# Optimization experiments

Measured on AMD Instinct MI355X. Metric: run time of the kernel, lower is better.

The kernel has to match this reference:

```python
import jax, jax.numpy as jnp
import numpy as np

N, DIM, H, W = 4, 64, 192, 192
K, DIL = 3, 1
STEP = DIL + 1
US = K + DIL * (K - 1)   # effective unfold window = 5
PAD = US // 2
EPS = 1e-5
D4 = DIM // 4


def group_norm(x, gamma, beta, groups=4, eps=EPS):
    n, c = x.shape[0], x.shape[1]
    xg = x.reshape(n, groups, -1)
    m = xg.mean(axis=2, keepdims=True)
    v = xg.var(axis=2, keepdims=True)
    xg = (xg - m) / jnp.sqrt(v + eps)
    xn = xg.reshape(x.shape)
    shp = (1, c) + (1,) * (x.ndim - 2)
    return xn * gamma.reshape(shp) + beta.reshape(shp)


def conv1x1(x, w, b):
    return jnp.einsum('nchw,oc->nohw', x, w) + b.reshape(1, -1, 1, 1)


def dwconv3(x, w, b, dilation):
    c = x.shape[1]
    p = dilation
    y = jax.lax.conv_general_dilated(x, w, (1, 1), [(p, p), (p, p)],
        rhs_dilation=(dilation, dilation), feature_group_count=c,
        dimension_numbers=('NCHW', 'OIHW', 'NCHW'))
    return y + b.reshape(1, -1, 1, 1)


def conv3(x, w, b):
    y = jax.lax.conv_general_dilated(x, w, (1, 1), [(1, 1), (1, 1)],
        dimension_numbers=('NCHW', 'OIHW', 'NCHW'))
    return y + b.reshape(1, -1, 1, 1)


def prelu(x, a):
    return jnp.where(x >= 0, x, a * x)


def forward(x, w_filter, gnf_g, gnf_b,
            lb_w1, lb_b1, lb_a1, lb_dw1, lb_db1,
            lb_w2, lb_b2, lb_a2, lb_dw2, lb_db2,
            lb_w3, lb_b3, lb_a3, lb_dw3, lb_db3,
            lb_w4, lb_b4, lb_a4, lb_w5, lb_b5,
            hb_gn_g, hb_gn_b, hb_w, hb_b,
            fu_w1, fu_b1, fu_gn_g, fu_gn_b, fu_w2, fu_b2):
    n, c, h, w = x.shape
    # dynamic per-channel filter from global average pool (1x1 spatial)
    fp = x.mean(axis=(2, 3))                          # [n, dim]
    fw = fp @ w_filter.T                              # 1x1 conv, no bias -> [n, dim*K*K]
    fw = group_norm(fw[:, :, None, None], gnf_g, gnf_b).reshape(n, DIM, K * K)
    fsm = jax.nn.softmax(fw, axis=2)                  # softmax over the K*K kernel taps
    # masked unfold == gather only the 9 dilated (stride-STEP) taps from reflect-padded x
    xp = jnp.pad(x, ((0, 0), (0, 0), (PAD, PAD), (PAD, PAD)), mode='reflect')
    taps = jnp.stack([xp[:, :, i:i + h, j:j + w]
                      for i in range(0, US, STEP)
                      for j in range(0, US, STEP)], axis=2)   # [n, dim, K*K, h, w]
    low = jnp.einsum('ndkhw,ndk->ndhw', taps, fsm)
    high = x - low
    # low-frequency branch
    y = prelu(conv1x1(low, lb_w1, lb_b1), lb_a1)
    y = dwconv3(y, lb_dw1, lb_db1, 5)
    y = prelu(conv1x1(y, lb_w2, lb_b2), lb_a2)
    y = dwconv3(y, lb_dw2, lb_db2, 1)
    y = prelu(conv1x1(y, lb_w3, lb_b3), lb_a3)
    y = dwconv3(y, lb_dw3, lb_db3, 3)
    y = prelu(conv1x1(y, lb_w4, lb_b4), lb_a4)
    enh_low = conv1x1(y, lb_w5, lb_b5)
    # high-frequency branch (GroupNorm -> LeakyReLU -> 3x3 conv) + residual
    z = group_norm(high, hb_gn_g, hb_gn_b)
    z = jnp.where(z >= 0, z, 0.01 * z)
    enh_high = conv3(z, hb_w, hb_b) + high
    # fusion
    fused = jnp.concatenate([enh_low, enh_high], axis=1)
    o = conv1x1(fused, fu_w1, fu_b1)
    o = group_norm(o, fu_gn_g, fu_gn_b)
    o = jax.nn.gelu(o, approximate=False)
    return conv1x1(o, fu_w2, fu_b2)


def setup_inputs():
    key = jax.random.key(0)
    ks = jax.random.split(key, 16)
    f32 = jnp.float32
    d, d4 = DIM, D4
    rn = lambda k, shape, s=0.05: jax.random.normal(k, shape, dtype=f32) * s
    a = lambda: jnp.array(0.25, f32)   # PReLU init
    return {
        'x': jax.random.normal(ks[0], (N, d, H, W), dtype=f32),
        'w_filter': rn(ks[1], (d * K * K, d)),
        'gnf_g': jnp.ones((d * K * K,), f32), 'gnf_b': jnp.zeros((d * K * K,), f32),
        'lb_w1': rn(ks[2], (d4, d)), 'lb_b1': jnp.zeros((d4,), f32), 'lb_a1': a(),
        'lb_dw1': rn(ks[3], (d4, 1, 3, 3)), 'lb_db1': jnp.zeros((d4,), f32),
        'lb_w2': rn(ks[4], (d4, d4)), 'lb_b2': jnp.zeros((d4,), f32), 'lb_a2': a(),
        'lb_dw2': rn(ks[5], (d4, 1, 3, 3)), 'lb_db2': jnp.zeros((d4,), f32),
        'lb_w3': rn(ks[6], (d4, d4)), 'lb_b3': jnp.zeros((d4,), f32), 'lb_a3': a(),
        'lb_dw3': rn(ks[7], (d4, 1, 3, 3)), 'lb_db3': jnp.zeros((d4,), f32),
        'lb_w4': rn(ks[8], (d4, d4)), 'lb_b4': jnp.zeros((d4,), f32), 'lb_a4': a(),
        'lb_w5': rn(ks[9], (d, d4)), 'lb_b5': jnp.zeros((d,), f32),
        'hb_gn_g': jnp.ones((d,), f32), 'hb_gn_b': jnp.zeros((d,), f32),
        'hb_w': rn(ks[10], (d, d, 3, 3)), 'hb_b': jnp.zeros((d,), f32),
        'fu_w1': rn(ks[11], (2 * d, 2 * d)), 'fu_b1': jnp.zeros((2 * d,), f32),
        'fu_gn_g': jnp.ones((2 * d,), f32), 'fu_gn_b': jnp.zeros((2 * d,), f32),
        'fu_w2': rn(ks[12], (d, 2 * d)), 'fu_b2': jnp.zeros((d,), f32),
    }


def reference(x, w_filter, gnf_g, gnf_b, lb_w1, lb_b1, lb_a1, lb_dw1, lb_db1, lb_w2, lb_b2, lb_a2, lb_dw2, lb_db2, lb_w3, lb_b3, lb_a3, lb_dw3, lb_db3, lb_w4, lb_b4, lb_a4, lb_w5, lb_b5, hb_gn_g, hb_gn_b, hb_w, hb_b, fu_w1, fu_b1, fu_gn_g, fu_gn_b, fu_w2, fu_b2):
    return forward(x, w_filter, gnf_g, gnf_b, lb_w1, lb_b1, lb_a1, lb_dw1, lb_db1, lb_w2, lb_b2, lb_a2, lb_dw2, lb_db2, lb_w3, lb_b3, lb_a3, lb_dw3, lb_db3, lb_w4, lb_b4, lb_a4, lb_w5, lb_b5, hb_gn_g, hb_gn_b, hb_w, hb_b, fu_w1, fu_b1, fu_gn_g, fu_gn_b, fu_w2, fu_b2)
```

## Files before the change

### kernel.cpp

```cpp
#include <hip/hip_runtime.h>
#include <hip/hip_bf16.h>
#include <math.h>

#define Nn 4
#define Cc 64
#define Hh 192
#define Ww 192
#define HW (Hh*Ww)
#define PIXBLK 144

typedef __attribute__((ext_vector_type(4))) float f32x4;
typedef __attribute__((ext_vector_type(8))) short s16x8;

struct __align__(8) US4 { unsigned short x,y,z,w; };

static __device__ __forceinline__ unsigned short f2bf(float v){
    __hip_bfloat16 b = __float2bfloat16(v);
    return *(unsigned short*)&b;
}
static __device__ __forceinline__ float bf2f(unsigned int u){
    return __uint_as_float(u<<16);
}

__global__ void k_prep(const float* __restrict__ hw, const float* __restrict__ fw1,
                       const float* __restrict__ fw2, const float* __restrict__ x,
                       unsigned short* __restrict__ g_wt,
                       unsigned short* __restrict__ g_wfu1,
                       unsigned short* __restrict__ g_wfu2,
                       float* __restrict__ fp){
    int b = blockIdx.x;
    __shared__ float sm[4];
    if(b < 240){
        int idx = b*256 + threadIdx.x;
        if(idx<36864){
            int og = idx/9216, r = idx%9216;
            int t = r/1024, r2 = r%1024;
            int o = r2>>6, c = r2&63;
            g_wt[idx] = f2bf(hw[(size_t)(((og*16+o)*64)+c)*9 + t]);
        } else if(idx<53248){
            int i = idx-36864;
            int o = i>>7, c = i&127;
            g_wfu1[o*128 + (c ^ ((o&15)<<3))] = f2bf(fw1[i]);
        } else {
            int i = idx-53248;
            int o = i>>7, c = i&127;
            g_wfu2[o*128 + (c ^ ((o&15)<<3))] = f2bf(fw2[i]);
        }
    } else {
        int nc = b-240;
        const float4* p = (const float4*)(x + (size_t)nc*HW);
        float s = 0.f;
        for(int i=threadIdx.x;i<HW/4;i+=256){ float4 v=p[i]; s += v.x+v.y+v.z+v.w; }
        for(int o=32;o>0;o>>=1) s += __shfl_down(s,o);
        int wid = threadIdx.x>>6, ln = threadIdx.x&63;
        if(ln==0) sm[wid]=s;
        __syncthreads();
        if(threadIdx.x==0) fp[nc] = (sm[0]+sm[1]+sm[2]+sm[3]) / (float)HW;
    }
}

__global__ void k_filter(const float* __restrict__ fp, const float* __restrict__ wf,
                         const float* __restrict__ gg, const float* __restrict__ gb,
                         float* __restrict__ fsm){
    int n = blockIdx.x;
    __shared__ float sfp[64];
    __shared__ float sfw[576];
    __shared__ float gstat[8];
    int t = threadIdx.x;
    if(t<64) sfp[t] = fp[n*64+t];
    __syncthreads();
    const float* wr = wf + (size_t)t*64;
    float acc = 0.f;
    #pragma unroll 8
    for(int k=0;k<64;k++) acc += sfp[k]*wr[k];
    sfw[t] = acc;
    __syncthreads();
    if(t<4){
        float s=0.f,s2=0.f;
        for(int i=0;i<144;i++){ float v=sfw[t*144+i]; s+=v; s2+=v*v; }
        float m = s/144.f;
        gstat[t*2]   = m;
        gstat[t*2+1] = s2/144.f - m*m;
    }
    __syncthreads();
    int g = t/144;
    float m = gstat[g*2], var = gstat[g*2+1];
    float z = (acc-m)*rsqrtf(var+1e-5f)*gg[t] + gb[t];
    sfw[t] = z;
    __syncthreads();
    if(t<64){
        float mx = -1e30f;
        for(int j=0;j<9;j++) mx = fmaxf(mx, sfw[t*9+j]);
        float e[9]; float se=0.f;
        for(int j=0;j<9;j++){ e[j]=expf(sfw[t*9+j]-mx); se+=e[j]; }
        float inv = 1.f/se;
        for(int j=0;j<9;j++) fsm[((size_t)n*64+t)*9+j] = e[j]*inv;
    }
}

#define HBS 88
__global__ void __launch_bounds__(256,3)
k_lowhigh(const float* __restrict__ x, const float* __restrict__ fsm,
          const float* __restrict__ w1, const float* __restrict__ b1,
          const float* __restrict__ a1p,
          unsigned short* __restrict__ high, float* __restrict__ y1,
          float* __restrict__ partial){
    int bid = blockIdx.x;
    int n = bid/144, tile = bid%144;
    int h0 = (tile/12)*16, w0 = (tile%12)*16;
    int t = threadIdx.x;
    int r0 = t>>4, wl = t&15;
    __shared__ __align__(16) unsigned short highbuf[256*HBS];
    __shared__ float sf[576];
    __shared__ float sw[1024];
    __shared__ float sb[16];
    __shared__ float redsm[4][8];
    for(int i=t;i<576;i+=256) sf[i] = fsm[(size_t)n*576+i];
    for(int i=t;i<1024;i+=256) sw[i] = w1[i];
    if(t<16) sb[t] = b1[t];
    __syncthreads();
    int rh[3], rw[3];
    #pragma unroll
    for(int k=0;k<3;k++){
        int a = h0 + r0 + 2*(k-1); if(a<0) a=-a; if(a>=Hh) a=2*(Hh-1)-a; rh[k]=a;
        int c = w0 + wl + 2*(k-1); if(c<0) c=-c; if(c>=Ww) c=2*(Ww-1)-c; rw[k]=c;
    }
    float acc[16];
    #pragma unroll
    for(int o=0;o<16;o++) acc[o]=0.f;
    const float* xb = x + (size_t)n*Cc*HW;
    int wv = t>>6, ln = t&63;
    #pragma unroll 1
    for(int grp=0; grp<4; grp++){
        float sg=0.f, sq=0.f;
        #pragma unroll 1
        for(int sub=0; sub<2; sub++){
            int oct = grp*2 + sub;
            unsigned int hp[4];
            #pragma unroll
            for(int j=0;j<8;j++){
                int c = oct*8 + j;
                const float* xc = xb + (size_t)c*HW;
                float low=0.f, ctr=0.f;
                #pragma unroll
                for(int ki=0;ki<3;ki++){
                    #pragma unroll
                    for(int kj=0;kj<3;kj++){
                        float v = xc[rh[ki]*Ww + rw[kj]];
                        low += sf[c*9 + ki*3 + kj]*v;
                        if(ki==1 && kj==1) ctr = v;
                    }
                }
                float hv = ctr-low;
                sg += hv; sq += hv*hv;
                unsigned short h16 = f2bf(hv);
                if(j&1) hp[j>>1] |= ((unsigned int)h16)<<16; else hp[j>>1] = h16;
                #pragma unroll
                for(int o=0;o<16;o++) acc[o] += sw[o*64+c]*low;
            }
            uint4 pk; pk.x=hp[0]; pk.y=hp[1]; pk.z=hp[2]; pk.w=hp[3];
            *(uint4*)&highbuf[t*HBS + oct*8] = pk;
        }
        #pragma unroll
        for(int o=32;o>0;o>>=1){ sg+=__shfl_down(sg,o); sq+=__shfl_down(sq,o); }
        if(ln==0){ redsm[wv][grp*2]=sg; redsm[wv][grp*2+1]=sq; }
    }
    float a1 = *a1p;
    #pragma unroll
    for(int o=0;o<16;o++){
        float v = acc[o] + sb[o];
        v = v>=0.f ? v : a1*v;
        y1[((size_t)n*16 + o)*HW + (h0+r0)*Ww + w0 + wl] = v;
    }
    __syncthreads();
    uint4* gout = (uint4*)(high + (size_t)n*HW*64);
    #pragma unroll
    for(int it=0;it<8;it++){
        int i = it*256 + t;
        int px = i>>3, sl = i&7;
        uint4 v = *(const uint4*)&highbuf[px*HBS + sl*8];
        gout[((size_t)(h0+(px>>4))*Ww + w0 + (px&15))*8 + sl] = v;
    }
    if(t<8) partial[(size_t)bid*8 + t] = redsm[0][t]+redsm[1][t]+redsm[2][t]+redsm[3][t];
}

template<int DILT>
__global__ void k_dw_c(const float* __restrict__ yin,
                       const float* __restrict__ dw, const float* __restrict__ db,
                       const float* __restrict__ wc, const float* __restrict__ bc,
                       const float* __restrict__ ap, float* __restrict__ yout){
    int bid = blockIdx.x;
    int n = bid/PIXBLK;
    int pix = (bid%PIXBLK)*256 + threadIdx.x;
    int h = pix/Ww, w = pix%Ww;
    __shared__ float sdw[16*9];
    __shared__ float swc[16*16];
    __shared__ float sdb[16], sbc[16];
    if(threadIdx.x<144) sdw[threadIdx.x] = dw[threadIdx.x];
    if(threadIdx.x>=144 && threadIdx.x<144+16){ sdb[threadIdx.x-144]=db[threadIdx.x-144]; }
    if(threadIdx.x>=160 && threadIdx.x<160+16){ sbc[threadIdx.x-160]=bc[threadIdx.x-160]; }
    for(int i=threadIdx.x;i<256;i+=256) swc[i]=wc[i];
    __syncthreads();
    float t16[16];
    const float* yb = yin + (size_t)n*16*HW;
    for(int c=0;c<16;c++){
        float s = 0.f;
        #pragma unroll
        for(int u=0;u<3;u++){
            int hh = h + DILT*(u-1);
            if(hh<0 || hh>=Hh) continue;
            #pragma unroll
            for(int v=0;v<3;v++){
                int wwi = w + DILT*(v-1);
                if(wwi<0 || wwi>=Ww) continue;
                s += yb[(size_t)c*HW + hh*Ww + wwi]*sdw[c*9+u*3+v];
            }
        }
        t16[c] = s + sdb[c];
    }
    float a = *ap;
    #pragma unroll
    for(int o=0;o<16;o++){
        float s = sbc[o];
        #pragma unroll
        for(int c=0;c<16;c++) s += swc[o*16+c]*t16[c];
        s = s>=0.f ? s : a*s;
        yout[((size_t)n*16 + o)*HW + pix] = s;
    }
}

__global__ void k_dw3_final(const float* __restrict__ yin,
                            const float* __restrict__ dw, const float* __restrict__ db,
                            const float* __restrict__ w4, const float* __restrict__ b4,
                            const float* __restrict__ a4p,
                            const float* __restrict__ w5, const float* __restrict__ b5,
                            unsigned short* __restrict__ enh_low){
    int bid = blockIdx.x;
    int n = bid/PIXBLK;
    int pix = (bid%PIXBLK)*256 + threadIdx.x;
    int h = pix/Ww, w = pix%Ww;
    __shared__ float sdw[16*9];
    __shared__ float sw4[16*16];
    __shared__ float sw5[64*16];
    __shared__ float sdb[16], sb4[16], sb5[64];
    if(threadIdx.x<144) sdw[threadIdx.x]=dw[threadIdx.x];
    if(threadIdx.x<16){ sdb[threadIdx.x]=db[threadIdx.x]; sb4[threadIdx.x]=b4[threadIdx.x]; }
    if(threadIdx.x<64) sb5[threadIdx.x]=b5[threadIdx.x];
    for(int i=threadIdx.x;i<256;i+=256) sw4[i]=w4[i];
    for(int i=threadIdx.x;i<1024;i+=256) sw5[i]=w5[i];
    __syncthreads();
    float t16[16];
    const float* yb = yin + (size_t)n*16*HW;
    for(int c=0;c<16;c++){
        float s=0.f;
        #pragma unroll
        for(int u=0;u<3;u++){
            int hh = h + 3*(u-1);
            if(hh<0||hh>=Hh) continue;
            #pragma unroll
            for(int v=0;v<3;v++){
                int wwi = w + 3*(v-1);
                if(wwi<0||wwi>=Ww) continue;
                s += yb[(size_t)c*HW + hh*Ww + wwi]*sdw[c*9+u*3+v];
            }
        }
        t16[c] = s + sdb[c];
    }
    float a = *a4p;
    float y4[16];
    #pragma unroll
    for(int o=0;o<16;o++){
        float s = sb4[o];
        #pragma unroll
        for(int c=0;c<16;c++) s += sw4[o*16+c]*t16[c];
        y4[o] = s>=0.f ? s : a*s;
    }
    unsigned short* dst = enh_low + ((size_t)n*HW + pix)*64;
    #pragma unroll
    for(int ob=0;ob<64;ob+=4){
        unsigned short tmp[4];
        #pragma unroll
        for(int j=0;j<4;j++){
            int o=ob+j;
            float s = sb5[o];
            #pragma unroll
            for(int c=0;c<16;c++) s += sw5[o*16+c]*y4[c];
            tmp[j]=f2bf(s);
        }
        US4 pk; pk.x=tmp[0]; pk.y=tmp[1]; pk.z=tmp[2]; pk.w=tmp[3];
        *(US4*)&dst[ob] = pk;
    }
}

__global__ void k_redstats(const float* __restrict__ partial, float* __restrict__ st, int nblk){
    int b = blockIdx.x;
    int n = b>>2, gl = b&3;
    int tid = threadIdx.x;
    float a0=0.f, a1=0.f;
    for(int pt=tid; pt<nblk; pt+=256){
        size_t base = (size_t)(n*nblk+pt)*8 + gl*2;
        a0 += partial[base];
        a1 += partial[base+1];
    }
    #pragma unroll
    for(int o=32;o>0;o>>=1){ a0+=__shfl_down(a0,o); a1+=__shfl_down(a1,o); }
    __shared__ float sm[8];
    int wv=tid>>6, ln=tid&63;
    if(ln==0){ sm[wv*2]=a0; sm[wv*2+1]=a1; }
    __syncthreads();
    if(tid==0){
        st[b*32+0] = sm[0]+sm[2]+sm[4]+sm[6];
        st[b*32+1] = sm[1]+sm[3]+sm[5]+sm[7];
    }
}

__global__ void __launch_bounds__(256,3)
k_conv3m(const unsigned short* __restrict__ high, const float* __restrict__ st,
         const float* __restrict__ gng, const float* __restrict__ gnb,
         const unsigned short* __restrict__ g_wt, const float* __restrict__ hb,
         unsigned short* __restrict__ enh_high){
    int bid = blockIdx.x;
    int n = bid/144, tile = bid%144;
    int tr0 = (tile/12)*16, tc0 = (tile%12)*16;
    __shared__ __align__(16) unsigned short z_lds[324*64];
    __shared__ float ssc[64], sbi[64], sbias[64];
    int tid = threadIdx.x;
    if(tid<64){
        int c=tid, g=n*4+(c>>4);
        float cnt=16.f*(float)HW;
        float m=st[g*32]/cnt, var=st[g*32+1]/cnt-m*m;
        float sc=gng[c]*rsqrtf(var+1e-5f);
        ssc[c]=sc; sbi[c]=gnb[c]-m*sc;
        sbias[c]=hb[c];
    }
    __syncthreads();
    const uint4* hpm = (const uint4*)(high + (size_t)n*HW*64);
    for(int e=tid;e<2592;e+=256){
        int hpx = e>>3, q = e&7;
        int hr = hpx/18, hc = hpx - hr*18;
        int gr = tr0+hr-1, gc = tc0+hc-1;
        uint4 w; w.x=0; w.y=0; w.z=0; w.w=0;
        if(gr>=0 && gr<Hh && gc>=0 && gc<Ww){
            uint4 v = hpm[(size_t)(gr*Ww+gc)*8 + q];
            unsigned int vv[4]={v.x,v.y,v.z,v.w};
            #pragma unroll
            for(int j=0;j<4;j++){
                int c = q*8 + 2*j;
                float f0 = bf2f(vv[j]&0xffffu)*ssc[c]   + sbi[c];
                float f1 = bf2f(vv[j]>>16)   *ssc[c+1] + sbi[c+1];
                f0 = f0>=0.f ? f0 : 0.01f*f0;
                f1 = f1>=0.f ? f1 : 0.01f*f1;
                vv[j] = (unsigned int)f2bf(f0) | ((unsigned int)f2bf(f1)<<16);
            }
            w.x=vv[0]; w.y=vv[1]; w.z=vv[2]; w.w=vv[3];
        }
        *(uint4*)&z_lds[hpx*64 + ((q*8) ^ ((hpx&7)<<3))] = w;
    }
    __syncthreads();
    int wv = tid>>6, ln = tid&63;
    int col = ln&15, kq = ln>>4;
    f32x4 acc[4][4];
    #pragma unroll
    for(int og=0;og<4;og++)
        #pragma unroll
        for(int rf=0;rf<4;rf++) acc[og][rf]=(f32x4){0.f,0.f,0.f,0.f};
    #pragma unroll
    for(int t=0;t<9;t++){
        int dr = t/3 - 1, dc = t%3 - 1;
        #pragma unroll
        for(int kb=0;kb<2;kb++){
            int k0 = kb*32 + kq*8;
            s16x8 afr[4];
            #pragma unroll
            for(int og=0;og<4;og++)
                afr[og] = *(const s16x8*)&g_wt[(size_t)(((og*9+t)*16+col)*64) + k0];
            #pragma unroll
            for(int rf=0;rf<4;rf++){
                int r = wv*4 + rf;
                int hpx = (r+1+dr)*18 + (col+1+dc);
                const s16x8 bfr = *(const s16x8*)&z_lds[hpx*64 + (k0 ^ ((hpx&7)<<3))];
                #pragma unroll
                for(int og=0;og<4;og++)
                    acc[og][rf] = __builtin_amdgcn_mfma_f32_16x16x32_bf16(afr[og], bfr, acc[og][rf], 0, 0, 0);
            }
        }
    }
    const unsigned short* hres = high + (size_t)n*HW*64;
    #pragma unroll
    for(int rf=0;rf<4;rf++){
        int r = wv*4 + rf;
        int gpx = (tr0+r)*Ww + (tc0+col);
        #pragma unroll
        for(int og=0;og<4;og++){
            US4 rv = *(const US4*)&hres[(size_t)gpx*64 + og*16 + kq*4];
            float rvf[4] = {bf2f(rv.x), bf2f(rv.y), bf2f(rv.z), bf2f(rv.w)};
            unsigned short tmp[4];
            #pragma unroll
            for(int reg=0;reg<4;reg++){
                int oc = og*16 + kq*4 + reg;
                tmp[reg] = f2bf(acc[og][rf][reg] + sbias[oc] + rvf[reg]);
            }
            US4 pk; pk.x=tmp[0]; pk.y=tmp[1]; pk.z=tmp[2]; pk.w=tmp[3];
            *(US4*)&enh_high[((size_t)n*HW + gpx)*64 + og*16 + kq*4] = pk;
        }
    }
}

__global__ void __launch_bounds__(256,2)
k_fu1m(const unsigned short* __restrict__ el, const unsigned short* __restrict__ eh,
       const unsigned short* __restrict__ wA, const float* __restrict__ b,
       unsigned short* __restrict__ o1, float* __restrict__ partial){
    int bid = blockIdx.x;
    int n = bid/288, pt = bid%288;
    int px0 = pt*128;
    __shared__ __align__(16) unsigned short sA[128*128];
    __shared__ __align__(16) unsigned short sB[128*128];
    __shared__ float sb[128];
    __shared__ float redsm[16];
    int tid = threadIdx.x;
    {
        const uint4* s=(const uint4*)wA; uint4* d=(uint4*)sA;
        for(int i=tid;i<2048;i+=256) d[i]=s[i];
    }
    if(tid<128) sb[tid]=b[tid];
    {
        const uint4* se=(const uint4*)(el + ((size_t)n*HW+px0)*64);
        const uint4* sh=(const uint4*)(eh + ((size_t)n*HW+px0)*64);
        for(int i=tid;i<2048;i+=256){
            int px=i>>4, q=i&15;
            uint4 v = (q<8)? se[px*8+q] : sh[px*8+(q-8)];
            int c0 = q*8;
            *(uint4*)&sB[px*128 + (c0 ^ ((px&15)<<3))] = v;
        }
    }
    __syncthreads();
    int wv=tid>>6, ln=tid&63;
    int wm=wv>>1, wn=wv&1;
    int col=ln&15, kq=ln>>4;
    f32x4 acc[4][4];
    #pragma unroll
    for(int m=0;m<4;m++)
        #pragma unroll
        for(int nf=0;nf<4;nf++) acc[m][nf]=(f32x4){0.f,0.f,0.f,0.f};
    #pragma unroll
    for(int kb=0;kb<4;kb++){
        int k0 = kb*32 + kq*8;
        s16x8 a[4], bf[4];
        #pragma unroll
        for(int m=0;m<4;m++)
            a[m] = *(const s16x8*)&sA[(wm*64+m*16+col)*128 + (k0 ^ (col<<3))];
        #pragma unroll
        for(int nf=0;nf<4;nf++)
            bf[nf] = *(const s16x8*)&sB[(wn*64+nf*16+col)*128 + (k0 ^ (col<<3))];
        #pragma unroll
        for(int m=0;m<4;m++)
            #pragma unroll
            for(int nf=0;nf<4;nf++)
                acc[m][nf] = __builtin_amdgcn_mfma_f32_16x16x32_bf16(a[m], bf[nf], acc[m][nf], 0,0,0);
    }
    float sg0=0.f,sq0=0.f,sg1=0.f,sq1=0.f;
    #pragma unroll
    for(int m=0;m<4;m++){
        int oc0 = wm*64 + m*16 + kq*4;
        #pragma unroll
        for(int nf=0;nf<4;nf++){
            int px = wn*64 + nf*16 + col;
            unsigned short tmp[4];
            #pragma unroll
            for(int reg=0;reg<4;reg++){
                float v = acc[m][nf][reg] + sb[oc0+reg];
                if(m<2){ sg0+=v; sq0+=v*v; } else { sg1+=v; sq1+=v*v; }
                tmp[reg]=f2bf(v);
            }
            US4 pk; pk.x=tmp[0]; pk.y=tmp[1]; pk.z=tmp[2]; pk.w=tmp[3];
            *(US4*)&o1[((size_t)n*HW + px0 + px)*128 + oc0] = pk;
        }
    }
    #pragma unroll
    for(int o=32;o>0;o>>=1){
        sg0+=__shfl_down(sg0,o); sq0+=__shfl_down(sq0,o);
        sg1+=__shfl_down(sg1,o); sq1+=__shfl_down(sq1,o);
    }
    if(ln==0){ redsm[wv*4+0]=sg0; redsm[wv*4+1]=sq0; redsm[wv*4+2]=sg1; redsm[wv*4+3]=sq1; }
    __syncthreads();
    if(tid<8){
        int gl = tid>>1, comp = tid&1;
        int wbase = (gl>>1)*2;
        int off = (gl&1)*2 + comp;
        partial[(size_t)bid*8 + tid] = redsm[wbase*4+off] + redsm[(wbase+1)*4+off];
    }
}

__global__ void __launch_bounds__(256,2)
k_fu2m(const unsigned short* __restrict__ o1, const float* __restrict__ st,
       const float* __restrict__ gg, const float* __restrict__ gb,
       const unsigned short* __restrict__ wA, const float* __restrict__ b2,
       float* __restrict__ out){
    int bid = blockIdx.x;
    int n = bid/288, pt = bid%288;
    int px0 = pt*128;
    __shared__ __align__(16) unsigned short sA[64*128];
    __shared__ __align__(16) unsigned short sB[128*128];
    __shared__ float ssc[128], sbi[128], sb2[64];
    int tid = threadIdx.x;
    {
        const uint4* s=(const uint4*)wA; uint4* d=(uint4*)sA;
        for(int i=tid;i<1024;i+=256) d[i]=s[i];
    }
    if(tid<128){
        int c=tid, g=n*4+(c>>5);
        float cnt = 32.f*(float)HW;
        float m = st[g*32]/cnt;
        float var = st[g*32+1]/cnt - m*m;
        float sc = gg[c]*rsqrtf(var+1e-5f);
        ssc[c]=sc; sbi[c]=gb[c]-m*sc;
    }
    if(tid<64) sb2[tid]=b2[tid];
    __syncthreads();
    {
        const uint4* so=(const uint4*)(o1 + ((size_t)n*HW+px0)*128);
        for(int i=tid;i<2048;i+=256){
            int px=i>>4, q=i&15;
            int c0 = q*8;
            uint4 v = so[px*16+q];
            unsigned int vals[4] = {v.x,v.y,v.z,v.w};
            #pragma unroll
            for(int j=0;j<4;j++){
                int c = c0 + 2*j;
                float f0 = bf2f(vals[j]&0xffffu)*ssc[c]   + sbi[c];
                float f1 = bf2f(vals[j]>>16)   *ssc[c+1] + sbi[c+1];
                f0 = 0.5f*f0*(1.f+erff(f0*0.70710678118654752f));
                f1 = 0.5f*f1*(1.f+erff(f1*0.70710678118654752f));
                vals[j] = (unsigned int)f2bf(f0) | ((unsigned int)f2bf(f1)<<16);
            }
            uint4 w; w.x=vals[0]; w.y=vals[1]; w.z=vals[2]; w.w=vals[3];
            *(uint4*)&sB[px*128 + (c0 ^ ((px&15)<<3))] = w;
        }
    }
    __syncthreads();
    int wv=tid>>6, ln=tid&63;
    int col=ln&15, kq=ln>>4;
    f32x4 acc[4][2];
    #pragma unroll
    for(int m=0;m<4;m++){ acc[m][0]=(f32x4){0,0,0,0}; acc[m][1]=(f32x4){0,0,0,0}; }
    #pragma unroll
    for(int kb=0;kb<4;kb++){
        int k0 = kb*32 + kq*8;
        s16x8 a[4], bf[2];
        #pragma unroll
        for(int m=0;m<4;m++)
            a[m] = *(const s16x8*)&sA[(m*16+col)*128 + (k0 ^ (col<<3))];
        #pragma unroll
        for(int nf=0;nf<2;nf++)
            bf[nf] = *(const s16x8*)&sB[(wv*32+nf*16+col)*128 + (k0 ^ (col<<3))];
        #pragma unroll
        for(int m=0;m<4;m++)
            #pragma unroll
            for(int nf=0;nf<2;nf++)
                acc[m][nf] = __builtin_amdgcn_mfma_f32_16x16x32_bf16(a[m], bf[nf], acc[m][nf], 0,0,0);
    }
    #pragma unroll
    for(int m=0;m<4;m++){
        int oc0 = m*16 + kq*4;
        #pragma unroll
        for(int nf=0;nf<2;nf++){
            int px = px0 + wv*32 + nf*16 + col;
            #pragma unroll
            for(int reg=0;reg<4;reg++){
                int oc = oc0+reg;
                out[((size_t)n*64+oc)*HW + px] = acc[m][nf][reg] + sb2[oc];
            }
        }
    }
}

extern "C" void kernel_launch(void* const* d_in, const int* in_sizes, int n_in,
                              void* d_out, int out_size, void* d_ws, size_t ws_size,
                              hipStream_t stream) {
    const float* x        = (const float*)d_in[0];
    const float* w_filter = (const float*)d_in[1];
    const float* gnf_g    = (const float*)d_in[2];
    const float* gnf_b    = (const float*)d_in[3];
    const float* lb_w1    = (const float*)d_in[4];
    const float* lb_b1    = (const float*)d_in[5];
    const float* lb_a1    = (const float*)d_in[6];
    const float* lb_dw1   = (const float*)d_in[7];
    const float* lb_db1   = (const float*)d_in[8];
    const float* lb_w2    = (const float*)d_in[9];
    const float* lb_b2    = (const float*)d_in[10];
    const float* lb_a2    = (const float*)d_in[11];
    const float* lb_dw2   = (const float*)d_in[12];
    const float* lb_db2   = (const float*)d_in[13];
    const float* lb_w3    = (const float*)d_in[14];
    const float* lb_b3    = (const float*)d_in[15];
    const float* lb_a3    = (const float*)d_in[16];
    const float* lb_dw3   = (const float*)d_in[17];
    const float* lb_db3   = (const float*)d_in[18];
    const float* lb_w4    = (const float*)d_in[19];
    const float* lb_b4    = (const float*)d_in[20];
    const float* lb_a4    = (const float*)d_in[21];
    const float* lb_w5    = (const float*)d_in[22];
    const float* lb_b5    = (const float*)d_in[23];
    const float* hb_gn_g  = (const float*)d_in[24];
    const float* hb_gn_b  = (const float*)d_in[25];
    const float* hb_w     = (const float*)d_in[26];
    const float* hb_b     = (const float*)d_in[27];
    const float* fu_w1    = (const float*)d_in[28];
    const float* fu_b1    = (const float*)d_in[29];
    const float* fu_gn_g  = (const float*)d_in[30];
    const float* fu_gn_b  = (const float*)d_in[31];
    const float* fu_w2    = (const float*)d_in[32];
    const float* fu_b2    = (const float*)d_in[33];
    float* out = (float*)d_out;

    const size_t O1B = (size_t)Nn*HW*128*2;
    const size_t EB  = (size_t)Nn*HW*64*2;
    const size_t YB  = (size_t)Nn*16*HW*4;
    char* Wb = (char*)d_ws;
    unsigned short* o1       = (unsigned short*)Wb;
    unsigned short* high     = (unsigned short*)Wb;
    unsigned short* enh_low  = (unsigned short*)(Wb + O1B);
    unsigned short* enh_high = (unsigned short*)(Wb + O1B + EB);
    float* y1                = (float*)(Wb + O1B + 2*EB);
    float* y2                = (float*)(Wb + O1B + 2*EB + YB);
    unsigned short* g_wt     = (unsigned short*)(Wb + O1B + 2*EB + 2*YB);
    unsigned short* g_wfu1   = g_wt + 36864;
    unsigned short* g_wfu2   = g_wfu1 + 16384;
    float* fp      = (float*)(g_wfu2 + 8192);
    float* fsm     = fp + 256;
    float* st_hb   = fsm + 2304;
    float* st_o1   = st_hb + 512;
    float* part_hb = st_o1 + 512;
    float* part_o1 = part_hb + 4608;

    k_prep<<<496, 256, 0, stream>>>(hb_w, fu_w1, fu_w2, x, g_wt, g_wfu1, g_wfu2, fp);
    k_filter<<<Nn, 576, 0, stream>>>(fp, w_filter, gnf_g, gnf_b, fsm);
    k_lowhigh<<<Nn*144, 256, 0, stream>>>(x, fsm, lb_w1, lb_b1, lb_a1, high, y1, part_hb);
    k_redstats<<<16, 256, 0, stream>>>(part_hb, st_hb, 144);
    k_conv3m<<<Nn*144, 256, 0, stream>>>(high, st_hb, hb_gn_g, hb_gn_b, g_wt, hb_b, enh_high);
    k_dw_c<5><<<Nn*PIXBLK, 256, 0, stream>>>(y1, lb_dw1, lb_db1, lb_w2, lb_b2, lb_a2, y2);
    k_dw_c<1><<<Nn*PIXBLK, 256, 0, stream>>>(y2, lb_dw2, lb_db2, lb_w3, lb_b3, lb_a3, y1);
    k_dw3_final<<<Nn*PIXBLK, 256, 0, stream>>>(y1, lb_dw3, lb_db3, lb_w4, lb_b4, lb_a4,
                                               lb_w5, lb_b5, enh_low);
    k_fu1m<<<Nn*288, 256, 0, stream>>>(enh_low, enh_high, g_wfu1, fu_b1, o1, part_o1);
    k_redstats<<<16, 256, 0, stream>>>(part_o1, st_o1, 288);
    k_fu2m<<<Nn*288, 256, 0, stream>>>(o1, st_o1, fu_gn_g, fu_gn_b, g_wfu2, fu_b2, out);
}
```

Baseline: 506.9 us.

## Convert input to channel-last bf16 and vectorise low/high tap gathers

Adds a pre-pass that transposes x from NCHW fp32 into NHWC bf16, so k_lowhigh can load 32 channels per tap with 16-byte vector loads instead of issuing scalar strided fp32 loads per channel. The tile shape changes from 16x16 to 8x32, and the 1x1 conv accumulation is restructured over 32-channel passes held in registers. This trades an extra full-tensor read/write pass and bf16 rounding of x (which affects the low/high values) for fewer, wider gathers. Register pressure rises, so launch bounds drop to 2 blocks per SM and the LDS pad shrinks.

```diff
diff --git a/kernel.cpp b/kernel.cpp
--- a/kernel.cpp
+++ b/kernel.cpp
@@ -20,6 +20,26 @@
 }
 static __device__ __forceinline__ float bf2f(unsigned int u){
     return __uint_as_float(u<<16);
+}
+
+__global__ void k_xprep(const float* __restrict__ x, unsigned short* __restrict__ xbf){
+    int bid = blockIdx.x;
+    int n = bid/144, chunk = bid%144;
+    int px = chunk*256 + threadIdx.x;
+    const float* xb = x + (size_t)n*Cc*HW + px;
+    unsigned int pk[32];
+    #pragma unroll
+    for(int c2=0;c2<32;c2++){
+        float f0 = xb[(size_t)(2*c2)*HW];
+        float f1 = xb[(size_t)(2*c2+1)*HW];
+        pk[c2] = (unsigned int)f2bf(f0) | ((unsigned int)f2bf(f1)<<16);
+    }
+    uint4* dst = (uint4*)(xbf + ((size_t)n*HW + px)*64);
+    #pragma unroll
+    for(int q=0;q<8;q++){
+        uint4 v; v.x=pk[q*4]; v.y=pk[q*4+1]; v.z=pk[q*4+2]; v.w=pk[q*4+3];
+        dst[q] = v;
+    }
 }
 
 __global__ void k_prep(const float* __restrict__ hw, const float* __restrict__ fw1,
@@ -98,18 +118,18 @@
     }
 }
 
-#define HBS 88
-__global__ void __launch_bounds__(256,3)
-k_lowhigh(const float* __restrict__ x, const float* __restrict__ fsm,
+#define HBS 72
+__global__ void __launch_bounds__(256,2)
+k_lowhigh(const unsigned short* __restrict__ xbf, const float* __restrict__ fsm,
           const float* __restrict__ w1, const float* __restrict__ b1,
           const float* __restrict__ a1p,
           unsigned short* __restrict__ high, float* __restrict__ y1,
           float* __restrict__ partial){
     int bid = blockIdx.x;
     int n = bid/144, tile = bid%144;
-    int h0 = (tile/12)*16, w0 = (tile%12)*16;
+    int h0 = (tile/6)*8, w0 = (tile%6)*32;
     int t = threadIdx.x;
-    int r0 = t>>4, wl = t&15;
+    int r0 = t>>5, wl = t&31;
     __shared__ __align__(16) unsigned short highbuf[256*HBS];
     __shared__ float sf[576];
     __shared__ float sw[1024];
@@ -125,45 +145,70 @@
         int a = h0 + r0 + 2*(k-1); if(a<0) a=-a; if(a>=Hh) a=2*(Hh-1)-a; rh[k]=a;
         int c = w0 + wl + 2*(k-1); if(c<0) c=-c; if(c>=Ww) c=2*(Ww-1)-c; rw[k]=c;
     }
+    const unsigned short* xb = xbf + (size_t)n*HW*64;
     float acc[16];
     #pragma unroll
     for(int o=0;o<16;o++) acc[o]=0.f;
-    const float* xb = x + (size_t)n*Cc*HW;
     int wv = t>>6, ln = t&63;
     #pragma unroll 1
-    for(int grp=0; grp<4; grp++){
-        float sg=0.f, sq=0.f;
-        #pragma unroll 1
-        for(int sub=0; sub<2; sub++){
-            int oct = grp*2 + sub;
+    for(int pass=0; pass<2; pass++){
+        float low[32];
+        #pragma unroll
+        for(int i=0;i<32;i++) low[i]=0.f;
+        uint4 c4[4];
+        #pragma unroll
+        for(int t9=0;t9<9;t9++){
+            int ki=t9/3, kj=t9%3;
+            const uint4* src = (const uint4*)(xb + ((size_t)(rh[ki]*Ww + rw[kj]))*64 + pass*32);
+            uint4 v4[4];
+            #pragma unroll
+            for(int q=0;q<4;q++) v4[q]=src[q];
+            if(t9==4){ c4[0]=v4[0]; c4[1]=v4[1]; c4[2]=v4[2]; c4[3]=v4[3]; }
+            #pragma unroll
+            for(int q=0;q<4;q++){
+                unsigned int vv[4]={v4[q].x,v4[q].y,v4[q].z,v4[q].w};
+                #pragma unroll
+                for(int j=0;j<4;j++){
+                    int lc = q*8 + 2*j;
+                    int c  = pass*32 + lc;
+                    low[lc]   += sf[c*9+t9]    *bf2f(vv[j]&0xffffu);
+                    low[lc+1] += sf[(c+1)*9+t9]*bf2f(vv[j]>>16);
+                }
+            }
+        }
+        float sg0=0.f,sq0=0.f,sg1=0.f,sq1=0.f;
+        #pragma unroll
+        for(int q=0;q<4;q++){
+            unsigned int vv[4]={c4[q].x,c4[q].y,c4[q].z,c4[q].w};
             unsigned int hp[4];
             #pragma unroll
-            for(int j=0;j<8;j++){
-                int c = oct*8 + j;
-                const float* xc = xb + (size_t)c*HW;
-                float low=0.f, ctr=0.f;
-                #pragma unroll
-                for(int ki=0;ki<3;ki++){
-                    #pragma unroll
-                    for(int kj=0;kj<3;kj++){
-                        float v = xc[rh[ki]*Ww + rw[kj]];
-                        low += sf[c*9 + ki*3 + kj]*v;
-                        if(ki==1 && kj==1) ctr = v;
-                    }
-                }
-                float hv = ctr-low;
-                sg += hv; sq += hv*hv;
-                unsigned short h16 = f2bf(hv);
-                if(j&1) hp[j>>1] |= ((unsigned int)h16)<<16; else hp[j>>1] = h16;
-                #pragma unroll
-                for(int o=0;o<16;o++) acc[o] += sw[o*64+c]*low;
+            for(int j=0;j<4;j++){
+                int lc = q*8 + 2*j;
+                float h0v = bf2f(vv[j]&0xffffu) - low[lc];
+                float h1v = bf2f(vv[j]>>16)     - low[lc+1];
+                if(q<2){ sg0+=h0v+h1v; sq0+=h0v*h0v+h1v*h1v; }
+                else   { sg1+=h0v+h1v; sq1+=h0v*h0v+h1v*h1v; }
+                hp[j] = (unsigned int)f2bf(h0v) | ((unsigned int)f2bf(h1v)<<16);
             }
             uint4 pk; pk.x=hp[0]; pk.y=hp[1]; pk.z=hp[2]; pk.w=hp[3];
-            *(uint4*)&highbuf[t*HBS + oct*8] = pk;
-        }
-        #pragma unroll
-        for(int o=32;o>0;o>>=1){ sg+=__shfl_down(sg,o); sq+=__shfl_down(sq,o); }
-        if(ln==0){ redsm[wv][grp*2]=sg; redsm[wv][grp*2+1]=sq; }
+            *(uint4*)&highbuf[t*HBS + (pass*4+q)*8] = pk;
+        }
+        #pragma unroll
+        for(int o=0;o<16;o++){
+            float s=0.f;
+            #pragma unroll
+            for(int lc=0;lc<32;lc++) s += sw[o*64 + pass*32 + lc]*low[lc];
+            acc[o] += s;
+        }
+        #pragma unroll
+        for(int o=32;o>0;o>>=1){
+            sg0+=__shfl_down(sg0,o); sq0+=__shfl_down(sq0,o);
+            sg1+=__shfl_down(sg1,o); sq1+=__shfl_down(sq1,o);
+        }
+        if(ln==0){
+            redsm[wv][pass*4+0]=sg0; redsm[wv][pass*4+1]=sq0;
+            redsm[wv][pass*4+2]=sg1; redsm[wv][pass*4+3]=sq1;
+        }
     }
     float a1 = *a1p;
     #pragma unroll
@@ -179,7 +224,7 @@
         int i = it*256 + t;
         int px = i>>3, sl = i&7;
         uint4 v = *(const uint4*)&highbuf[px*HBS + sl*8];
-        gout[((size_t)(h0+(px>>4))*Ww + w0 + (px&15))*8 + sl] = v;
+        gout[((size_t)(h0+(px>>5))*Ww + w0 + (px&31))*8 + sl] = v;
     }
     if(t<8) partial[(size_t)bid*8 + t] = redsm[0][t]+redsm[1][t]+redsm[2][t]+redsm[3][t];
 }
@@ -632,10 +677,12 @@
     float* st_o1   = st_hb + 512;
     float* part_hb = st_o1 + 512;
     float* part_o1 = part_hb + 4608;
-
+    unsigned short* xbf = (unsigned short*)(part_o1 + 9216);
+
+    k_xprep<<<Nn*144, 256, 0, stream>>>(x, xbf);
     k_prep<<<496, 256, 0, stream>>>(hb_w, fu_w1, fu_w2, x, g_wt, g_wfu1, g_wfu2, fp);
     k_filter<<<Nn, 576, 0, stream>>>(fp, w_filter, gnf_g, gnf_b, fsm);
-    k_lowhigh<<<Nn*144, 256, 0, stream>>>(x, fsm, lb_w1, lb_b1, lb_a1, high, y1, part_hb);
+    k_lowhigh<<<Nn*144, 256, 0, stream>>>(xbf, fsm, lb_w1, lb_b1, lb_a1, high, y1, part_hb);
     k_redstats<<<16, 256, 0, stream>>>(part_hb, st_hb, 144);
     k_conv3m<<<Nn*144, 256, 0, stream>>>(high, st_hb, hb_gn_g, hb_gn_b, g_wt, hb_b, enh_high);
     k_dw_c<5><<<Nn*PIXBLK, 256, 0, stream>>>(y1, lb_dw1, lb_db1, lb_w2, lb_b2, lb_a2, y2);
```

New measurement: 713.8 us. 40.8% more time.

## Convert x to channel-last bf16 and vectorize low/high tap gathers

Applied to the files above, without the earlier changes.

Adds a kernel that transposes x from NCHW fp32 into NHWC bf16, so k_lowhigh can load eight channels per tap with a single 16-byte load instead of 72 strided scalar fp32 loads. The tile shape changes to 8x32, the highbuf padding is reduced, and the launch bounds drop to 2 blocks per SM. Low-pass and high-pass values are now computed from bf16-rounded inputs, which lowers precision. The new pass also costs an extra read and write of x.

```diff
diff --git a/kernel.cpp b/kernel.cpp
--- a/kernel.cpp
+++ b/kernel.cpp
@@ -20,6 +20,26 @@
 }
 static __device__ __forceinline__ float bf2f(unsigned int u){
     return __uint_as_float(u<<16);
+}
+
+__global__ void k_xprep(const float* __restrict__ x, unsigned short* __restrict__ xbf){
+    int bid = blockIdx.x;
+    int n = bid/144, chunk = bid%144;
+    int px = chunk*256 + threadIdx.x;
+    const float* xb = x + (size_t)n*Cc*HW + px;
+    unsigned int pk[32];
+    #pragma unroll
+    for(int c2=0;c2<32;c2++){
+        float f0 = xb[(size_t)(2*c2)*HW];
+        float f1 = xb[(size_t)(2*c2+1)*HW];
+        pk[c2] = (unsigned int)f2bf(f0) | ((unsigned int)f2bf(f1)<<16);
+    }
+    uint4* dst = (uint4*)(xbf + ((size_t)n*HW + px)*64);
+    #pragma unroll
+    for(int q=0;q<8;q++){
+        uint4 v; v.x=pk[q*4]; v.y=pk[q*4+1]; v.z=pk[q*4+2]; v.w=pk[q*4+3];
+        dst[q] = v;
+    }
 }
 
 __global__ void k_prep(const float* __restrict__ hw, const float* __restrict__ fw1,
@@ -98,18 +118,18 @@
     }
 }
 
-#define HBS 88
-__global__ void __launch_bounds__(256,3)
-k_lowhigh(const float* __restrict__ x, const float* __restrict__ fsm,
+#define HBS 72
+__global__ void __launch_bounds__(256,2)
+k_lowhigh(const unsigned short* __restrict__ xbf, const float* __restrict__ fsm,
           const float* __restrict__ w1, const float* __restrict__ b1,
           const float* __restrict__ a1p,
           unsigned short* __restrict__ high, float* __restrict__ y1,
           float* __restrict__ partial){
     int bid = blockIdx.x;
     int n = bid/144, tile = bid%144;
-    int h0 = (tile/12)*16, w0 = (tile%12)*16;
+    int h0 = (tile/6)*8, w0 = (tile%6)*32;
     int t = threadIdx.x;
-    int r0 = t>>4, wl = t&15;
+    int r0 = t>>5, wl = t&31;
     __shared__ __align__(16) unsigned short highbuf[256*HBS];
     __shared__ float sf[576];
     __shared__ float sw[1024];
@@ -119,57 +139,71 @@
     for(int i=t;i<1024;i+=256) sw[i] = w1[i];
     if(t<16) sb[t] = b1[t];
     __syncthreads();
-    int rh[3], rw[3];
-    #pragma unroll
-    for(int k=0;k<3;k++){
-        int a = h0 + r0 + 2*(k-1); if(a<0) a=-a; if(a>=Hh) a=2*(Hh-1)-a; rh[k]=a;
-        int c = w0 + wl + 2*(k-1); if(c<0) c=-c; if(c>=Ww) c=2*(Ww-1)-c; rw[k]=c;
-    }
+    int a0=h0+r0-2, a1=h0+r0, a2=h0+r0+2;
+    if(a0<0)a0=-a0; if(a2>=Hh)a2=2*(Hh-1)-a2;
+    int c0w=w0+wl-2, c1w=w0+wl, c2w=w0+wl+2;
+    if(c0w<0)c0w=-c0w; if(c2w>=Ww)c2w=2*(Ww-1)-c2w;
+    const unsigned short* xb = xbf + (size_t)n*HW*64;
+    size_t tp0=((size_t)a0*Ww+c0w)*8, tp1=((size_t)a0*Ww+c1w)*8, tp2=((size_t)a0*Ww+c2w)*8;
+    size_t tp3=((size_t)a1*Ww+c0w)*8, tp4=((size_t)a1*Ww+c1w)*8, tp5=((size_t)a1*Ww+c2w)*8;
+    size_t tp6=((size_t)a2*Ww+c0w)*8, tp7=((size_t)a2*Ww+c1w)*8, tp8=((size_t)a2*Ww+c2w)*8;
+    const uint4* xq = (const uint4*)xb;
     float acc[16];
     #pragma unroll
     for(int o=0;o<16;o++) acc[o]=0.f;
-    const float* xb = x + (size_t)n*Cc*HW;
     int wv = t>>6, ln = t&63;
     #pragma unroll 1
     for(int grp=0; grp<4; grp++){
         float sg=0.f, sq=0.f;
-        #pragma unroll 1
+        #pragma unroll
         for(int sub=0; sub<2; sub++){
-            int oct = grp*2 + sub;
-            unsigned int hp[4];
-            #pragma unroll
-            for(int j=0;j<8;j++){
-                int c = oct*8 + j;
-                const float* xc = xb + (size_t)c*HW;
-                float low=0.f, ctr=0.f;
-                #pragma unroll
-                for(int ki=0;ki<3;ki++){
-                    #pragma unroll
-                    for(int kj=0;kj<3;kj++){
-                        float v = xc[rh[ki]*Ww + rw[kj]];
-                        low += sf[c*9 + ki*3 + kj]*v;
-                        if(ki==1 && kj==1) ctr = v;
-                    }
-                }
-                float hv = ctr-low;
-                sg += hv; sq += hv*hv;
-                unsigned short h16 = f2bf(hv);
-                if(j&1) hp[j>>1] |= ((unsigned int)h16)<<16; else hp[j>>1] = h16;
-                #pragma unroll
-                for(int o=0;o<16;o++) acc[o] += sw[o*64+c]*low;
-            }
-            uint4 pk; pk.x=hp[0]; pk.y=hp[1]; pk.z=hp[2]; pk.w=hp[3];
+            const int oct = grp*2+sub;
+            float l0=0,l1=0,l2=0,l3=0,l4=0,l5=0,l6=0,l7=0;
+            unsigned int cx=0,cy=0,cz=0,cw=0;
+            const float* sfo = &sf[oct*8*9];
+            #pragma unroll
+            for(int t9=0;t9<9;t9++){
+                size_t tb = (t9==0)?tp0:(t9==1)?tp1:(t9==2)?tp2:(t9==3)?tp3:
+                            (t9==4)?tp4:(t9==5)?tp5:(t9==6)?tp6:(t9==7)?tp7:tp8;
+                const uint4 v = xq[tb + oct];
+                if(t9==4){ cx=v.x; cy=v.y; cz=v.z; cw=v.w; }
+                l0 += sfo[0*9+t9]*bf2f(v.x&0xffffu);
+                l1 += sfo[1*9+t9]*bf2f(v.x>>16);
+                l2 += sfo[2*9+t9]*bf2f(v.y&0xffffu);
+                l3 += sfo[3*9+t9]*bf2f(v.y>>16);
+                l4 += sfo[4*9+t9]*bf2f(v.z&0xffffu);
+                l5 += sfo[5*9+t9]*bf2f(v.z>>16);
+                l6 += sfo[6*9+t9]*bf2f(v.w&0xffffu);
+                l7 += sfo[7*9+t9]*bf2f(v.w>>16);
+            }
+            float h0v=bf2f(cx&0xffffu)-l0, h1v=bf2f(cx>>16)-l1;
+            float h2v=bf2f(cy&0xffffu)-l2, h3v=bf2f(cy>>16)-l3;
+            float h4v=bf2f(cz&0xffffu)-l4, h5v=bf2f(cz>>16)-l5;
+            float h6v=bf2f(cw&0xffffu)-l6, h7v=bf2f(cw>>16)-l7;
+            sg += h0v+h1v+h2v+h3v+h4v+h5v+h6v+h7v;
+            sq += h0v*h0v+h1v*h1v+h2v*h2v+h3v*h3v+h4v*h4v+h5v*h5v+h6v*h6v+h7v*h7v;
+            uint4 pk;
+            pk.x = (unsigned int)f2bf(h0v) | ((unsigned int)f2bf(h1v)<<16);
+            pk.y = (unsigned int)f2bf(h2v) | ((unsigned int)f2bf(h3v)<<16);
+            pk.z = (unsigned int)f2bf(h4v) | ((unsigned int)f2bf(h5v)<<16);
+            pk.w = (unsigned int)f2bf(h6v) | ((unsigned int)f2bf(h7v)<<16);
             *(uint4*)&highbuf[t*HBS + oct*8] = pk;
+            const float* swo = &sw[oct*8];
+            #pragma unroll
+            for(int o=0;o<16;o++){
+                acc[o] += swo[o*64+0]*l0 + swo[o*64+1]*l1 + swo[o*64+2]*l2 + swo[o*64+3]*l3
+                        + swo[o*64+4]*l4 + swo[o*64+5]*l5 + swo[o*64+6]*l6 + swo[o*64+7]*l7;
+            }
         }
         #pragma unroll
         for(int o=32;o>0;o>>=1){ sg+=__shfl_down(sg,o); sq+=__shfl_down(sq,o); }
         if(ln==0){ redsm[wv][grp*2]=sg; redsm[wv][grp*2+1]=sq; }
     }
-    float a1 = *a1p;
+    float a1p_ = *a1p;
     #pragma unroll
     for(int o=0;o<16;o++){
         float v = acc[o] + sb[o];
-        v = v>=0.f ? v : a1*v;
+        v = v>=0.f ? v : a1p_*v;
         y1[((size_t)n*16 + o)*HW + (h0+r0)*Ww + w0 + wl] = v;
     }
     __syncthreads();
@@ -179,7 +213,7 @@
         int i = it*256 + t;
         int px = i>>3, sl = i&7;
         uint4 v = *(const uint4*)&highbuf[px*HBS + sl*8];
-        gout[((size_t)(h0+(px>>4))*Ww + w0 + (px&15))*8 + sl] = v;
+        gout[((size_t)(h0+(px>>5))*Ww + w0 + (px&31))*8 + sl] = v;
     }
     if(t<8) partial[(size_t)bid*8 + t] = redsm[0][t]+redsm[1][t]+redsm[2][t]+redsm[3][t];
 }
@@ -632,10 +666,12 @@
     float* st_o1   = st_hb + 512;
     float* part_hb = st_o1 + 512;
     float* part_o1 = part_hb + 4608;
-
+    unsigned short* xbf = (unsigned short*)(part_o1 + 9216);
+
+    k_xprep<<<Nn*144, 256, 0, stream>>>(x, xbf);
     k_prep<<<496, 256, 0, stream>>>(hb_w, fu_w1, fu_w2, x, g_wt, g_wfu1, g_wfu2, fp);
     k_filter<<<Nn, 576, 0, stream>>>(fp, w_filter, gnf_g, gnf_b, fsm);
-    k_lowhigh<<<Nn*144, 256, 0, stream>>>(x, fsm, lb_w1, lb_b1, lb_a1, high, y1, part_hb);
+    k_lowhigh<<<Nn*144, 256, 0, stream>>>(xbf, fsm, lb_w1, lb_b1, lb_a1, high, y1, part_hb);
     k_redstats<<<16, 256, 0, stream>>>(part_hb, st_hb, 144);
     k_conv3m<<<Nn*144, 256, 0, stream>>>(high, st_hb, hb_gn_g, hb_gn_b, g_wt, hb_b, enh_high);
     k_dw_c<5><<<Nn*PIXBLK, 256, 0, stream>>>(y1, lb_dw1, lb_db1, lb_w2, lb_b2, lb_a2, y2);
```

Result: slower. 540.9 us (+6.7%).
